# Optimization experiments

Measured on AMD Instinct MI355X. Metric: run time of the kernel, lower is better.

The kernel has to match this reference:

```python
import jax, jax.numpy as jnp
import numpy as np

HEADS = 8
DIM_HEAD = 64
BN_EPS = 1e-5

def setup_inputs() -> dict:
    key = jax.random.key(0)
    ks = jax.random.split(key, 6)
    B, N, D = 8, 1024, 512
    inner = HEADS * DIM_HEAD  # 512
    return {
        "x": jax.random.normal(ks[0], (B, N, D), dtype=jnp.float32),
        "w_qkv": jax.random.normal(ks[1], (D, 3 * inner), dtype=jnp.float32) * (D ** -0.5),
        "conv_w": jax.random.normal(ks[2], (HEADS, HEADS), dtype=jnp.float32) * (HEADS ** -0.5),
        "conv_b": jax.random.normal(ks[3], (HEADS,), dtype=jnp.float32) * 0.02,
        "bn_gamma": jnp.ones((HEADS,), dtype=jnp.float32),
        "bn_beta": jnp.zeros((HEADS,), dtype=jnp.float32),
        "w_out": jax.random.normal(ks[4], (inner, D), dtype=jnp.float32) * (inner ** -0.5),
        "b_out": jnp.zeros((D,), dtype=jnp.float32),
    }

def reference(x, w_qkv, conv_w, conv_b, bn_gamma, bn_beta, w_out, b_out):
    B, N, D = x.shape
    H, dh = HEADS, DIM_HEAD
    scale = dh ** -0.5
    qkv = x @ w_qkv  # [B, N, 3*H*dh]
    q, k, v = jnp.split(qkv, 3, axis=-1)
    # b n (h d) -> b h n d
    q = q.reshape(B, N, H, dh).transpose(0, 2, 1, 3)
    k = k.reshape(B, N, H, dh).transpose(0, 2, 1, 3)
    v = v.reshape(B, N, H, dh).transpose(0, 2, 1, 3)
    attn = jnp.einsum('bhnd,bhmd->bhnm', q, k) * scale
    attn = jax.nn.softmax(attn, axis=-1)
    # 1x1 conv across heads (channels = heads)
    attn = jnp.einsum('gh,bhnm->bgnm', conv_w, attn) + conv_b[None, :, None, None]
    # BatchNorm2d in training mode: batch stats over (B, N, N) per head, biased variance
    mean = attn.mean(axis=(0, 2, 3), keepdims=True)
    var = attn.var(axis=(0, 2, 3), keepdims=True)
    attn = (attn - mean) * jax.lax.rsqrt(var + BN_EPS)
    attn = attn * bn_gamma[None, :, None, None] + bn_beta[None, :, None, None]
    # reatten_scale = 1.0 (transform_scale=False)
    out = jnp.einsum('bhnm,bhmd->bhnd', attn, v)
    out = out.transpose(0, 2, 1, 3).reshape(B, N, H * dh)  # b h n d -> b n (h d)
    return out @ w_out + b_out
```

## Files before the change

kernel.cpp:

```cpp
#include <hip/hip_runtime.h>
#include <math.h>


#define Bz 8
#define Nn 1024
#define Dd 512
#define Hh 8
#define DH 64
#define INNER 512
#define QW 1536
#define SCALE 0.125f
#define BN_EPS 1e-5f

typedef short bf16x8 __attribute__((ext_vector_type(8)));
typedef float f32x4 __attribute__((ext_vector_type(4)));

#define MFMA(a, b, c) __builtin_amdgcn_mfma_f32_16x16x32_bf16((a), (b), (c), 0, 0, 0)

__device__ __forceinline__ unsigned short f2b(float f) {
  union { float f; unsigned u; } v; v.f = f;
  unsigned r = v.u + 0x7fffu + ((v.u >> 16) & 1u);
  return (unsigned short)(r >> 16);
}
__device__ __forceinline__ float b2f(unsigned short s) {
  union { unsigned u; float f; } v; v.u = ((unsigned)s) << 16;
  return v.f;
}

#define WB_QKV 0u
#define WB_VT (WB_QKV + 25165824u)
#define WB_WQT (WB_VT + 8388608u)
#define WB_WOT (WB_WQT + 1572864u)
#define WB_O1 (WB_WOT + 524288u)
#define WB_VSUM (WB_O1 + 16777216u)
#define WB_STATS (WB_VSUM + 16384u)
#define WB_AC (WB_STATS + 64u)

__global__ __launch_bounds__(256) void k_transpose(const float* __restrict__ src,
                                                   unsigned short* __restrict__ dst,
                                                   int R, int C) {
  __shared__ float tile[32][33];
  const int tc = blockIdx.x * 32, tr = blockIdx.y * 32;
  const int lx = threadIdx.x & 31, ly = threadIdx.x >> 5;
#pragma unroll
  for (int i = 0; i < 32; i += 8)
    tile[ly + i][lx] = src[(size_t)(tr + ly + i) * C + tc + lx];
  __syncthreads();
#pragma unroll
  for (int i = 0; i < 32; i += 8)
    dst[(size_t)(tc + ly + i) * R + tr + lx] = f2b(tile[lx][ly + i]);
}

__global__ __launch_bounds__(256) void k_qkv(const float* __restrict__ X,
                                             const unsigned short* __restrict__ WQT,
                                             unsigned short* __restrict__ qkv,
                                             unsigned short* __restrict__ vT) {
  __shared__ unsigned short sA[128][40];
  __shared__ unsigned short sB[128][40];
  const int t = threadIdx.x;
  const int col0 = blockIdx.x * 128;
  const int row0 = blockIdx.y * 128;
  const int l = t & 63, w = t >> 6;
  const int wm = (w & 1) * 64, wn = (w >> 1) * 64;
  const int lm = l & 15, lq = l >> 4;
  const int srow = t >> 1, skc = (t & 1) * 16;
  f32x4 acc[4][4] = {};
  for (int k0 = 0; k0 < Dd; k0 += 32) {
    {
      const float* src = X + (size_t)(row0 + srow) * Dd + k0 + skc;
      unsigned short tmp[16];
#pragma unroll
      for (int c4 = 0; c4 < 4; c4++) {
        float4 f = *(const float4*)(src + c4 * 4);
        tmp[c4 * 4 + 0] = f2b(f.x);
        tmp[c4 * 4 + 1] = f2b(f.y);
        tmp[c4 * 4 + 2] = f2b(f.z);
        tmp[c4 * 4 + 3] = f2b(f.w);
      }
      *(uint4*)&sA[srow][skc] = *(uint4*)tmp;
      *(uint4*)&sA[srow][skc + 8] = *(uint4*)(tmp + 8);
    }
    {
      const unsigned short* srcB = WQT + (size_t)(col0 + srow) * Dd + k0 + skc;
      *(uint4*)&sB[srow][skc] = *(const uint4*)srcB;
      *(uint4*)&sB[srow][skc + 8] = *(const uint4*)(srcB + 8);
    }
    __syncthreads();
    bf16x8 af[4], bfr[4];
#pragma unroll
    for (int i = 0; i < 4; i++) af[i] = *(const bf16x8*)&sA[wm + 16 * i + lm][lq * 8];
#pragma unroll
    for (int j = 0; j < 4; j++) bfr[j] = *(const bf16x8*)&sB[wn + 16 * j + lm][lq * 8];
#pragma unroll
    for (int i = 0; i < 4; i++)
#pragma unroll
      for (int j = 0; j < 4; j++) acc[i][j] = MFMA(af[i], bfr[j], acc[i][j]);
    __syncthreads();
  }
  const bool isv = (col0 >= 2 * INNER);
#pragma unroll
  for (int i = 0; i < 4; i++) {
    const int rbase = row0 + wm + 16 * i + lq * 4;
#pragma unroll
    for (int j = 0; j < 4; j++) {
      const int col = col0 + wn + 16 * j + lm;
#pragma unroll
      for (int r = 0; r < 4; r++) {
        unsigned short hv = f2b(acc[i][j][r]);
        const int row = rbase + r;
        if (!isv) {
          qkv[(size_t)row * QW + col] = hv;
        } else {
          const int b = row >> 10, mseq = row & 1023;
          const int gd = col - 2 * INNER;
          vT[(((size_t)(b * Hh + (gd >> 6))) * DH + (gd & 63)) * Nn + mseq] = hv;
        }
      }
    }
  }
}

__global__ __launch_bounds__(256) void k_vsum(const unsigned short* __restrict__ vT,
                                              float* __restrict__ vsum) {
  const int bg = blockIdx.x;
  const int d = threadIdx.x >> 2, qq = threadIdx.x & 3;
  __shared__ float red[64][4];
  const unsigned short* p = vT + ((size_t)bg * DH + d) * Nn + qq * 256;
  float s = 0.f;
  for (int m = 0; m < 256; m += 4) {
    uint2 rr = *(const uint2*)(p + m);
    s += b2f((unsigned short)(rr.x & 0xffff)) + b2f((unsigned short)(rr.x >> 16)) +
         b2f((unsigned short)(rr.y & 0xffff)) + b2f((unsigned short)(rr.y >> 16));
  }
  red[d][qq] = s;
  __syncthreads();
  if (threadIdx.x < 64)
    vsum[(size_t)bg * DH + threadIdx.x] =
        red[threadIdx.x][0] + red[threadIdx.x][1] + red[threadIdx.x][2] + red[threadIdx.x][3];
}

__global__ __launch_bounds__(512, 2) void k_attn(const unsigned short* __restrict__ qkv,
                                                 const unsigned short* __restrict__ vT,
                                                 const float* __restrict__ conv_w,
                                                 float* __restrict__ O1,
                                                 float* __restrict__ stats) {
  __shared__ unsigned short sQ[8][32][88];
  __shared__ unsigned short sKV[22528];
  __shared__ float sS[8][32][36];
  __shared__ unsigned short sU[8][32][40];
  __shared__ float sRinv[8][32];
  __shared__ float sRed[8][16];
  const int b = blockIdx.x;
  const int n0 = blockIdx.y * 32;
  const int t = threadIdx.x;
  const int w = t >> 6, l = t & 63;
  const int lm = l & 15, lq = l >> 4;
  float cw[64];
#pragma unroll
  for (int i = 0; i < 64; i++) cw[i] = conv_w[i];

  {
    const int row = t >> 1, kc = (t & 1) * 32;
    const int h = row >> 5, n = row & 31;
    const unsigned short* src = qkv + (size_t)(b * Nn + n0 + n) * QW + h * DH + kc;
    uint4 v0 = *(const uint4*)src, v1 = *(const uint4*)(src + 8);
    uint4 v2 = *(const uint4*)(src + 16), v3 = *(const uint4*)(src + 24);
    *(uint4*)&sQ[h][n][kc] = v0;
    *(uint4*)&sQ[h][n][kc + 8] = v1;
    *(uint4*)&sQ[h][n][kc + 16] = v2;
    *(uint4*)&sQ[h][n][kc + 24] = v3;
  }
  __syncthreads();

  float psum[2][4] = {};
  for (int m0 = 0; m0 < Nn; m0 += 32) {
    {
      const int row = t >> 1, kc = (t & 1) * 32;
      const int h = row >> 5, m = row & 31;
      const unsigned short* src = qkv + (size_t)(b * Nn + m0 + m) * QW + INNER + h * DH + kc;
      unsigned short* dst = &sKV[(h * 32 + m) * 88 + kc];
      uint4 v0 = *(const uint4*)src, v1 = *(const uint4*)(src + 8);
      uint4 v2 = *(const uint4*)(src + 16), v3 = *(const uint4*)(src + 24);
      *(uint4*)dst = v0;
      *(uint4*)(dst + 8) = v1;
      *(uint4*)(dst + 16) = v2;
      *(uint4*)(dst + 24) = v3;
    }
    __syncthreads();
    f32x4 lac[2][2] = {};
#pragma unroll
    for (int ks = 0; ks < 2; ks++) {
      bf16x8 a0 = *(const bf16x8*)&sQ[w][lm][ks * 32 + lq * 8];
      bf16x8 a1 = *(const bf16x8*)&sQ[w][16 + lm][ks * 32 + lq * 8];
      bf16x8 b0 = *(const bf16x8*)&sKV[(w * 32 + lm) * 88 + ks * 32 + lq * 8];
      bf16x8 b1 = *(const bf16x8*)&sKV[(w * 32 + 16 + lm) * 88 + ks * 32 + lq * 8];
      lac[0][0] = MFMA(a0, b0, lac[0][0]);
      lac[0][1] = MFMA(a0, b1, lac[0][1]);
      lac[1][0] = MFMA(a1, b0, lac[1][0]);
      lac[1][1] = MFMA(a1, b1, lac[1][1]);
    }
    __syncthreads();
#pragma unroll
    for (int i = 0; i < 2; i++)
#pragma unroll
      for (int j = 0; j < 2; j++)
#pragma unroll
        for (int r = 0; r < 4; r++) psum[i][r] += __expf(lac[i][j][r] * SCALE);
  }
#pragma unroll
  for (int i = 0; i < 2; i++)
#pragma unroll
    for (int r = 0; r < 4; r++) {
      float s = psum[i][r];
      s += __shfl_xor(s, 1);
      s += __shfl_xor(s, 2);
      s += __shfl_xor(s, 4);
      s += __shfl_xor(s, 8);
      if (lm == 0) sRinv[w][16 * i + lq * 4 + r] = 1.0f / s;
    }
  __syncthreads();
  float rv[2][4];
#pragma unroll
  for (int i = 0; i < 2; i++)
#pragma unroll
    for (int r = 0; r < 4; r++) rv[i][r] = sRinv[w][16 * i + lq * 4 + r];

  f32x4 oacc[2][4] = {};
  float su[8] = {}, su2[8] = {};
  const int mxn = t >> 4;
  const int mxm = (t & 15) * 2;
  for (int m0 = 0; m0 < Nn; m0 += 32) {
    {
      const int row = t >> 1, kc = (t & 1) * 32;
      const int h = row >> 5, m = row & 31;
      const unsigned short* src = qkv + (size_t)(b * Nn + m0 + m) * QW + INNER + h * DH + kc;
      unsigned short* dst = &sKV[(h * 32 + m) * 88 + kc];
      uint4 v0 = *(const uint4*)src, v1 = *(const uint4*)(src + 8);
      uint4 v2 = *(const uint4*)(src + 16), v3 = *(const uint4*)(src + 24);
      *(uint4*)dst = v0;
      *(uint4*)(dst + 8) = v1;
      *(uint4*)(dst + 16) = v2;
      *(uint4*)(dst + 24) = v3;
    }
    __syncthreads();
    f32x4 lac[2][2] = {};
#pragma unroll
    for (int ks = 0; ks < 2; ks++) {
      bf16x8 a0 = *(const bf16x8*)&sQ[w][lm][ks * 32 + lq * 8];
      bf16x8 a1 = *(const bf16x8*)&sQ[w][16 + lm][ks * 32 + lq * 8];
      bf16x8 b0 = *(const bf16x8*)&sKV[(w * 32 + lm) * 88 + ks * 32 + lq * 8];
      bf16x8 b1 = *(const bf16x8*)&sKV[(w * 32 + 16 + lm) * 88 + ks * 32 + lq * 8];
      lac[0][0] = MFMA(a0, b0, lac[0][0]);
      lac[0][1] = MFMA(a0, b1, lac[0][1]);
      lac[1][0] = MFMA(a1, b0, lac[1][0]);
      lac[1][1] = MFMA(a1, b1, lac[1][1]);
    }
#pragma unroll
    for (int i = 0; i < 2; i++)
#pragma unroll
      for (int j = 0; j < 2; j++)
#pragma unroll
        for (int r = 0; r < 4; r++)
          sS[w][16 * i + lq * 4 + r][16 * j + lm] = __expf(lac[i][j][r] * SCALE) * rv[i][r];
    __syncthreads();
    {
      const unsigned short* src = vT + ((size_t)(b * Hh + (t >> 6)) * DH + (t & 63)) * Nn + m0;
      unsigned short* dst = &sKV[((t >> 6) * 64 + (t & 63)) * 40];
      uint4 v0 = *(const uint4*)src, v1 = *(const uint4*)(src + 8);
      uint4 v2 = *(const uint4*)(src + 16), v3 = *(const uint4*)(src + 24);
      *(uint4*)dst = v0;
      *(uint4*)(dst + 8) = v1;
      *(uint4*)(dst + 16) = v2;
      *(uint4*)(dst + 24) = v3;
    }
    {
      float2 sv[8];
#pragma unroll
      for (int h = 0; h < 8; h++) sv[h] = *(const float2*)&sS[h][mxn][mxm];
#pragma unroll
      for (int g = 0; g < 8; g++) {
        float u0 = 0.f, u1 = 0.f;
#pragma unroll
        for (int h = 0; h < 8; h++) {
          u0 += cw[g * 8 + h] * sv[h].x;
          u1 += cw[g * 8 + h] * sv[h].y;
        }
        su[g] += u0 + u1;
        su2[g] += u0 * u0 + u1 * u1;
        unsigned pk = (unsigned)f2b(u0) | ((unsigned)f2b(u1) << 16);
        *(unsigned*)&sU[g][mxn][mxm] = pk;
      }
    }
    __syncthreads();
    {
      bf16x8 ua0 = *(const bf16x8*)&sU[w][lm][lq * 8];
      bf16x8 ua1 = *(const bf16x8*)&sU[w][16 + lm][lq * 8];
#pragma unroll
      for (int j = 0; j < 4; j++) {
        bf16x8 vb = *(const bf16x8*)&sKV[(w * 64 + 16 * j + lm) * 40 + lq * 8];
        oacc[0][j] = MFMA(ua0, vb, oacc[0][j]);
        oacc[1][j] = MFMA(ua1, vb, oacc[1][j]);
      }
    }
    __syncthreads();
  }
#pragma unroll
  for (int i = 0; i < 2; i++) {
    const int n = n0 + 16 * i + lq * 4;
#pragma unroll
    for (int j = 0; j < 4; j++) {
      float* dst = O1 + (((size_t)(b * Hh + w)) * Nn + n) * DH + 16 * j + lm;
#pragma unroll
      for (int r = 0; r < 4; r++) dst[(size_t)r * DH] = oacc[i][j][r];
    }
  }
#pragma unroll
  for (int g = 0; g < 8; g++) {
    float a = su[g], q = su2[g];
    for (int off = 32; off; off >>= 1) {
      a += __shfl_down(a, off);
      q += __shfl_down(q, off);
    }
    if (l == 0) {
      sRed[w][g] = a;
      sRed[w][8 + g] = q;
    }
  }
  __syncthreads();
  if (t < 16) {
    float s = 0.f;
#pragma unroll
    for (int ww = 0; ww < 8; ww++) s += sRed[ww][t];
    atomicAdd(&stats[t], s);
  }
}

__global__ void k_alpha(const float* __restrict__ stats, const float* __restrict__ bn_gamma,
                        const float* __restrict__ bn_beta, float* __restrict__ ac) {
  const int g = threadIdx.x;
  if (g < 8) {
    const float cnt = (float)Bz * (float)Nn * (float)Nn;
    float Eu = stats[g] / cnt;
    float Eu2 = stats[8 + g] / cnt;
    float inv = rsqrtf(Eu2 - Eu * Eu + BN_EPS);
    float alpha = bn_gamma[g] * inv;
    ac[g] = alpha;
    ac[8 + g] = bn_beta[g] - Eu * alpha;
  }
}

__global__ __launch_bounds__(256) void k_out(const float* __restrict__ O1,
                                             const float* __restrict__ vsum,
                                             const float* __restrict__ ac,
                                             const unsigned short* __restrict__ WOT,
                                             const float* __restrict__ bout,
                                             float* __restrict__ out) {
  __shared__ unsigned short sA[128][40];
  __shared__ unsigned short sB[128][40];
  __shared__ float sAl[16];
  const int t = threadIdx.x;
  if (t < 16) sAl[t] = ac[t];
  const int col0 = blockIdx.x * 128, row0 = blockIdx.y * 128;
  const int l = t & 63, w = t >> 6;
  const int wm = (w & 1) * 64, wn = (w >> 1) * 64;
  const int lm = l & 15, lq = l >> 4;
  const int srow = t >> 1, skc = (t & 1) * 16;
  const int b = row0 >> 10;
  const int nn = (row0 + srow) & 1023;
  f32x4 acc[4][4] = {};
  __syncthreads();
  for (int k0 = 0; k0 < INNER; k0 += 32) {
    {
      const int k = k0 + skc;
      const int g = k >> 6, dd = k & 63;
      const float al = sAl[g], cc = sAl[8 + g];
      const float* op = O1 + (((size_t)(b * Hh + g)) * Nn + nn) * DH + dd;
      const float* vp = vsum + ((size_t)(b * Hh + g)) * DH + dd;
      unsigned short tmp[16];
#pragma unroll
      for (int c4 = 0; c4 < 4; c4++) {
        float4 o4 = *(const float4*)(op + c4 * 4);
        float4 v4 = *(const float4*)(vp + c4 * 4);
        tmp[c4 * 4 + 0] = f2b(al * o4.x + cc * v4.x);
        tmp[c4 * 4 + 1] = f2b(al * o4.y + cc * v4.y);
        tmp[c4 * 4 + 2] = f2b(al * o4.z + cc * v4.z);
        tmp[c4 * 4 + 3] = f2b(al * o4.w + cc * v4.w);
      }
      *(uint4*)&sA[srow][skc] = *(uint4*)tmp;
      *(uint4*)&sA[srow][skc + 8] = *(uint4*)(tmp + 8);
    }
    {
      const unsigned short* srcB = WOT + (size_t)(col0 + srow) * INNER + k0 + skc;
      *(uint4*)&sB[srow][skc] = *(const uint4*)srcB;
      *(uint4*)&sB[srow][skc + 8] = *(const uint4*)(srcB + 8);
    }
    __syncthreads();
    bf16x8 af[4], bfr[4];
#pragma unroll
    for (int i = 0; i < 4; i++) af[i] = *(const bf16x8*)&sA[wm + 16 * i + lm][lq * 8];
#pragma unroll
    for (int j = 0; j < 4; j++) bfr[j] = *(const bf16x8*)&sB[wn + 16 * j + lm][lq * 8];
#pragma unroll
    for (int i = 0; i < 4; i++)
#pragma unroll
      for (int j = 0; j < 4; j++) acc[i][j] = MFMA(af[i], bfr[j], acc[i][j]);
    __syncthreads();
  }
#pragma unroll
  for (int j = 0; j < 4; j++) {
    const int col = col0 + wn + 16 * j + lm;
    const float bo = bout[col];
#pragma unroll
    for (int i = 0; i < 4; i++) {
      const int rbase = row0 + wm + 16 * i + lq * 4;
#pragma unroll
      for (int r = 0; r < 4; r++) out[(size_t)(rbase + r) * Dd + col] = acc[i][j][r] + bo;
    }
  }
}

extern "C" void kernel_launch(void* const* d_in, const int* in_sizes, int n_in,
                              void* d_out, int out_size, void* d_ws, size_t ws_size,
                              hipStream_t stream) {
  const float* x = (const float*)d_in[0];
  const float* w_qkv = (const float*)d_in[1];
  const float* conv_w = (const float*)d_in[2];
  const float* bn_gamma = (const float*)d_in[4];
  const float* bn_beta = (const float*)d_in[5];
  const float* w_out = (const float*)d_in[6];
  const float* b_out = (const float*)d_in[7];
  char* ws = (char*)d_ws;
  unsigned short* QKV = (unsigned short*)(ws + WB_QKV);
  unsigned short* VT = (unsigned short*)(ws + WB_VT);
  unsigned short* WQT = (unsigned short*)(ws + WB_WQT);
  unsigned short* WOT = (unsigned short*)(ws + WB_WOT);
  float* O1 = (float*)(ws + WB_O1);
  float* VSUM = (float*)(ws + WB_VSUM);
  float* STATS = (float*)(ws + WB_STATS);
  float* AC = (float*)(ws + WB_AC);

  hipMemsetAsync(STATS, 0, 64, stream);
  k_transpose<<<dim3(48, 16), 256, 0, stream>>>(w_qkv, WQT, 512, 1536);
  k_transpose<<<dim3(16, 16), 256, 0, stream>>>(w_out, WOT, 512, 512);
  k_qkv<<<dim3(12, 64), 256, 0, stream>>>(x, WQT, QKV, VT);
  k_vsum<<<64, 256, 0, stream>>>(VT, VSUM);
  k_attn<<<dim3(8, 32), 512, 0, stream>>>(QKV, VT, conv_w, O1, STATS);
  k_alpha<<<1, 64, 0, stream>>>(STATS, bn_gamma, bn_beta, AC);
  k_out<<<dim3(4, 64), 256, 0, stream>>>(O1, VSUM, AC, WOT, b_out, (float*)d_out);
}
```

Baseline: 317.6 us.

## Split attention into score-materializing kernel and head-mixing SV kernel

The fused attention kernel, which computed QK^T twice (once for row sums, once for probabilities), is replaced by two kernels. The first writes unnormalized exp scores in bf16 to a 128MB global buffer together with reciprocal row sums. The second reads those scores, applies the head-mixing conv and accumulates into O1 and the BN statistics. The QKV GEMM epilogue also stages results through shared memory so global stores are coalesced, including the transposed V output. The cost is large global memory traffic for the score buffer in exchange for removing the duplicated QK matmul and getting better occupancy.

```diff
diff --git a/kernel.cpp b/kernel.cpp
--- a/kernel.cpp
+++ b/kernel.cpp
@@ -32,7 +32,9 @@
 #define WB_WQT (WB_VT + 8388608u)
 #define WB_WOT (WB_WQT + 1572864u)
 #define WB_O1 (WB_WOT + 524288u)
-#define WB_VSUM (WB_O1 + 16777216u)
+#define WB_SG (WB_O1 + 16777216u)
+#define WB_RINV (WB_SG + 134217728u)
+#define WB_VSUM (WB_RINV + 262144u)
 #define WB_STATS (WB_VSUM + 16384u)
 #define WB_AC (WB_STATS + 64u)
 
@@ -55,11 +57,14 @@
                                              const unsigned short* __restrict__ WQT,
                                              unsigned short* __restrict__ qkv,
                                              unsigned short* __restrict__ vT) {
-  __shared__ unsigned short sA[128][40];
-  __shared__ unsigned short sB[128][40];
+  extern __shared__ char smem[];
+  unsigned short(*sA)[40] = (unsigned short(*)[40])smem;
+  unsigned short(*sB)[40] = (unsigned short(*)[40])(smem + 128 * 40 * 2);
+  unsigned short* sEp = (unsigned short*)smem;
   const int t = threadIdx.x;
   const int col0 = blockIdx.x * 128;
   const int row0 = blockIdx.y * 128;
+  const bool isqk = (col0 < 2 * INNER);
   const int l = t & 63, w = t >> 6;
   const int wm = (w & 1) * 64, wn = (w >> 1) * 64;
   const int lm = l & 15, lq = l >> 4;
@@ -91,32 +96,54 @@
     for (int i = 0; i < 4; i++) af[i] = *(const bf16x8*)&sA[wm + 16 * i + lm][lq * 8];
 #pragma unroll
     for (int j = 0; j < 4; j++) bfr[j] = *(const bf16x8*)&sB[wn + 16 * j + lm][lq * 8];
-#pragma unroll
-    for (int i = 0; i < 4; i++)
-#pragma unroll
-      for (int j = 0; j < 4; j++) acc[i][j] = MFMA(af[i], bfr[j], acc[i][j]);
-    __syncthreads();
-  }
-  const bool isv = (col0 >= 2 * INNER);
-#pragma unroll
-  for (int i = 0; i < 4; i++) {
-    const int rbase = row0 + wm + 16 * i + lq * 4;
-#pragma unroll
-    for (int j = 0; j < 4; j++) {
-      const int col = col0 + wn + 16 * j + lm;
-#pragma unroll
-      for (int r = 0; r < 4; r++) {
-        unsigned short hv = f2b(acc[i][j][r]);
-        const int row = rbase + r;
-        if (!isv) {
-          qkv[(size_t)row * QW + col] = hv;
-        } else {
-          const int b = row >> 10, mseq = row & 1023;
-          const int gd = col - 2 * INNER;
-          vT[(((size_t)(b * Hh + (gd >> 6))) * DH + (gd & 63)) * Nn + mseq] = hv;
-        }
-      }
-    }
+    if (isqk) {
+#pragma unroll
+      for (int i = 0; i < 4; i++)
+#pragma unroll
+        for (int j = 0; j < 4; j++) acc[i][j] = MFMA(bfr[i], af[j], acc[i][j]);
+    } else {
+#pragma unroll
+      for (int i = 0; i < 4; i++)
+#pragma unroll
+        for (int j = 0; j < 4; j++) acc[i][j] = MFMA(af[i], bfr[j], acc[i][j]);
+    }
+    __syncthreads();
+  }
+  if (isqk) {
+#pragma unroll
+    for (int jc = 0; jc < 4; jc++)
+#pragma unroll
+      for (int ir = 0; ir < 4; ir++) {
+        unsigned short us[4];
+#pragma unroll
+        for (int r = 0; r < 4; r++) us[r] = f2b(acc[jc][ir][r]);
+        *(uint2*)&sEp[(wm + 16 * ir + lm) * 136 + wn + 16 * jc + 4 * lq] = *(uint2*)us;
+      }
+    __syncthreads();
+    const int row = t >> 1, half = t & 1;
+    const unsigned short* src = &sEp[row * 136 + half * 64];
+    unsigned short* dst = qkv + (size_t)(row0 + row) * QW + col0 + half * 64;
+#pragma unroll
+    for (int c = 0; c < 8; c++) *(uint4*)(dst + c * 8) = *(const uint4*)(src + c * 8);
+  } else {
+#pragma unroll
+    for (int ir = 0; ir < 4; ir++)
+#pragma unroll
+      for (int jc = 0; jc < 4; jc++) {
+        unsigned short us[4];
+#pragma unroll
+        for (int r = 0; r < 4; r++) us[r] = f2b(acc[ir][jc][r]);
+        *(uint2*)&sEp[(wn + 16 * jc + lm) * 136 + wm + 16 * ir + 4 * lq] = *(uint2*)us;
+      }
+    __syncthreads();
+    const int row = t >> 1, half = t & 1;
+    const int gd = col0 - 2 * INNER + row;
+    const int bq = row0 >> 10, mseq0 = row0 & 1023;
+    const unsigned short* src = &sEp[row * 136 + half * 64];
+    unsigned short* dst =
+        vT + (((size_t)(bq * Hh + (gd >> 6)) * DH + (gd & 63)) << 10) + mseq0 + half * 64;
+#pragma unroll
+    for (int c = 0; c < 8; c++) *(uint4*)(dst + c * 8) = *(const uint4*)(src + c * 8);
   }
 }
 
@@ -139,181 +166,132 @@
         red[threadIdx.x][0] + red[threadIdx.x][1] + red[threadIdx.x][2] + red[threadIdx.x][3];
 }
 
-__global__ __launch_bounds__(512, 2) void k_attn(const unsigned short* __restrict__ qkv,
-                                                 const unsigned short* __restrict__ vT,
-                                                 const float* __restrict__ conv_w,
-                                                 float* __restrict__ O1,
-                                                 float* __restrict__ stats) {
-  __shared__ unsigned short sQ[8][32][88];
-  __shared__ unsigned short sKV[22528];
-  __shared__ float sS[8][32][36];
-  __shared__ unsigned short sU[8][32][40];
-  __shared__ float sRinv[8][32];
-  __shared__ float sRed[8][16];
-  const int b = blockIdx.x;
-  const int n0 = blockIdx.y * 32;
+__global__ __launch_bounds__(512, 4) void k_sgen(const unsigned short* __restrict__ qkv,
+                                                 unsigned short* __restrict__ Sg,
+                                                 float* __restrict__ rinvG) {
+  __shared__ unsigned short sK[64 * 80];
+  __shared__ unsigned short sSout[128 * 72];
+  const int b = blockIdx.x, ntile = blockIdx.y, h = blockIdx.z;
+  const int n0 = ntile * 128;
   const int t = threadIdx.x;
   const int w = t >> 6, l = t & 63;
   const int lm = l & 15, lq = l >> 4;
+  bf16x8 qf[2];
+  {
+    const unsigned short* qp =
+        qkv + (size_t)(b * Nn + n0 + w * 16 + lm) * QW + h * DH + lq * 8;
+    qf[0] = *(const bf16x8*)(qp);
+    qf[1] = *(const bf16x8*)(qp + 32);
+  }
+  float psum = 0.f;
+  for (int m0 = 0; m0 < Nn; m0 += 64) {
+    {
+      const int row = t >> 3, c = (t & 7) * 8;
+      *(uint4*)&sK[row * 80 + c] =
+          *(const uint4*)(qkv + (size_t)(b * Nn + m0 + row) * QW + INNER + h * DH + c);
+    }
+    __syncthreads();
+    f32x4 lac[4] = {};
+#pragma unroll
+    for (int j = 0; j < 4; j++) {
+      bf16x8 a0 = *(const bf16x8*)&sK[(16 * j + lm) * 80 + lq * 8];
+      bf16x8 a1 = *(const bf16x8*)&sK[(16 * j + lm) * 80 + 32 + lq * 8];
+      lac[j] = MFMA(a0, qf[0], lac[j]);
+      lac[j] = MFMA(a1, qf[1], lac[j]);
+    }
+#pragma unroll
+    for (int j = 0; j < 4; j++) {
+      unsigned short us[4];
+#pragma unroll
+      for (int r = 0; r < 4; r++) {
+        float e = __expf(lac[j][r] * SCALE);
+        psum += e;
+        us[r] = f2b(e);
+      }
+      *(uint2*)&sSout[(w * 16 + lm) * 72 + 16 * j + 4 * lq] = *(uint2*)us;
+    }
+    __syncthreads();
+    {
+      const int row = t >> 2, c = (t & 3) * 16;
+      const unsigned short* src = &sSout[row * 72 + c];
+      unsigned short* dst =
+          Sg + ((size_t)(b * Hh + h) << 20) + (size_t)(n0 + row) * Nn + m0 + c;
+      *(uint4*)dst = *(const uint4*)src;
+      *(uint4*)(dst + 8) = *(const uint4*)(src + 8);
+    }
+  }
+  psum += __shfl_xor(psum, 16);
+  psum += __shfl_xor(psum, 32);
+  if (lq == 0) rinvG[(size_t)(b * Hh + h) * Nn + n0 + w * 16 + lm] = 1.0f / psum;
+}
+
+__global__ __launch_bounds__(512, 4) void k_mixsv(const unsigned short* __restrict__ Sg,
+                                                  const unsigned short* __restrict__ vT,
+                                                  const float* __restrict__ rinvG,
+                                                  const float* __restrict__ conv_w,
+                                                  float* __restrict__ O1,
+                                                  float* __restrict__ stats) {
+  __shared__ unsigned short sU[8 * 16 * 72];
+  __shared__ float sRed[8][16];
+  const int b = blockIdx.x;
+  const int n0 = blockIdx.y * 16;
+  const int t = threadIdx.x;
+  const int w = t >> 6, l = t & 63;
+  const int lm = l & 15, lq = l >> 4;
+  const int mxn = t >> 5, mxm = (t & 31) * 2;
   float cw[64];
 #pragma unroll
   for (int i = 0; i < 64; i++) cw[i] = conv_w[i];
-
-  {
-    const int row = t >> 1, kc = (t & 1) * 32;
-    const int h = row >> 5, n = row & 31;
-    const unsigned short* src = qkv + (size_t)(b * Nn + n0 + n) * QW + h * DH + kc;
-    uint4 v0 = *(const uint4*)src, v1 = *(const uint4*)(src + 8);
-    uint4 v2 = *(const uint4*)(src + 16), v3 = *(const uint4*)(src + 24);
-    *(uint4*)&sQ[h][n][kc] = v0;
-    *(uint4*)&sQ[h][n][kc + 8] = v1;
-    *(uint4*)&sQ[h][n][kc + 16] = v2;
-    *(uint4*)&sQ[h][n][kc + 24] = v3;
-  }
-  __syncthreads();
-
-  float psum[2][4] = {};
-  for (int m0 = 0; m0 < Nn; m0 += 32) {
-    {
-      const int row = t >> 1, kc = (t & 1) * 32;
-      const int h = row >> 5, m = row & 31;
-      const unsigned short* src = qkv + (size_t)(b * Nn + m0 + m) * QW + INNER + h * DH + kc;
-      unsigned short* dst = &sKV[(h * 32 + m) * 88 + kc];
-      uint4 v0 = *(const uint4*)src, v1 = *(const uint4*)(src + 8);
-      uint4 v2 = *(const uint4*)(src + 16), v3 = *(const uint4*)(src + 24);
-      *(uint4*)dst = v0;
-      *(uint4*)(dst + 8) = v1;
-      *(uint4*)(dst + 16) = v2;
-      *(uint4*)(dst + 24) = v3;
-    }
-    __syncthreads();
-    f32x4 lac[2][2] = {};
-#pragma unroll
-    for (int ks = 0; ks < 2; ks++) {
-      bf16x8 a0 = *(const bf16x8*)&sQ[w][lm][ks * 32 + lq * 8];
-      bf16x8 a1 = *(const bf16x8*)&sQ[w][16 + lm][ks * 32 + lq * 8];
-      bf16x8 b0 = *(const bf16x8*)&sKV[(w * 32 + lm) * 88 + ks * 32 + lq * 8];
-      bf16x8 b1 = *(const bf16x8*)&sKV[(w * 32 + 16 + lm) * 88 + ks * 32 + lq * 8];
-      lac[0][0] = MFMA(a0, b0, lac[0][0]);
-      lac[0][1] = MFMA(a0, b1, lac[0][1]);
-      lac[1][0] = MFMA(a1, b0, lac[1][0]);
-      lac[1][1] = MFMA(a1, b1, lac[1][1]);
-    }
-    __syncthreads();
-#pragma unroll
-    for (int i = 0; i < 2; i++)
-#pragma unroll
-      for (int j = 0; j < 2; j++)
-#pragma unroll
-        for (int r = 0; r < 4; r++) psum[i][r] += __expf(lac[i][j][r] * SCALE);
-  }
-#pragma unroll
-  for (int i = 0; i < 2; i++)
-#pragma unroll
-    for (int r = 0; r < 4; r++) {
-      float s = psum[i][r];
-      s += __shfl_xor(s, 1);
-      s += __shfl_xor(s, 2);
-      s += __shfl_xor(s, 4);
-      s += __shfl_xor(s, 8);
-      if (lm == 0) sRinv[w][16 * i + lq * 4 + r] = 1.0f / s;
-    }
-  __syncthreads();
-  float rv[2][4];
-#pragma unroll
-  for (int i = 0; i < 2; i++)
-#pragma unroll
-    for (int r = 0; r < 4; r++) rv[i][r] = sRinv[w][16 * i + lq * 4 + r];
-
-  f32x4 oacc[2][4] = {};
+  float rv[8];
+#pragma unroll
+  for (int h = 0; h < 8; h++) rv[h] = rinvG[(size_t)(b * Hh + h) * Nn + n0 + mxn];
+  f32x4 oacc[4] = {};
   float su[8] = {}, su2[8] = {};
-  const int mxn = t >> 4;
-  const int mxm = (t & 15) * 2;
-  for (int m0 = 0; m0 < Nn; m0 += 32) {
-    {
-      const int row = t >> 1, kc = (t & 1) * 32;
-      const int h = row >> 5, m = row & 31;
-      const unsigned short* src = qkv + (size_t)(b * Nn + m0 + m) * QW + INNER + h * DH + kc;
-      unsigned short* dst = &sKV[(h * 32 + m) * 88 + kc];
-      uint4 v0 = *(const uint4*)src, v1 = *(const uint4*)(src + 8);
-      uint4 v2 = *(const uint4*)(src + 16), v3 = *(const uint4*)(src + 24);
-      *(uint4*)dst = v0;
-      *(uint4*)(dst + 8) = v1;
-      *(uint4*)(dst + 16) = v2;
-      *(uint4*)(dst + 24) = v3;
-    }
-    __syncthreads();
-    f32x4 lac[2][2] = {};
-#pragma unroll
-    for (int ks = 0; ks < 2; ks++) {
-      bf16x8 a0 = *(const bf16x8*)&sQ[w][lm][ks * 32 + lq * 8];
-      bf16x8 a1 = *(const bf16x8*)&sQ[w][16 + lm][ks * 32 + lq * 8];
-      bf16x8 b0 = *(const bf16x8*)&sKV[(w * 32 + lm) * 88 + ks * 32 + lq * 8];
-      bf16x8 b1 = *(const bf16x8*)&sKV[(w * 32 + 16 + lm) * 88 + ks * 32 + lq * 8];
-      lac[0][0] = MFMA(a0, b0, lac[0][0]);
-      lac[0][1] = MFMA(a0, b1, lac[0][1]);
-      lac[1][0] = MFMA(a1, b0, lac[1][0]);
-      lac[1][1] = MFMA(a1, b1, lac[1][1]);
-    }
-#pragma unroll
-    for (int i = 0; i < 2; i++)
-#pragma unroll
-      for (int j = 0; j < 2; j++)
-#pragma unroll
-        for (int r = 0; r < 4; r++)
-          sS[w][16 * i + lq * 4 + r][16 * j + lm] = __expf(lac[i][j][r] * SCALE) * rv[i][r];
-    __syncthreads();
-    {
-      const unsigned short* src = vT + ((size_t)(b * Hh + (t >> 6)) * DH + (t & 63)) * Nn + m0;
-      unsigned short* dst = &sKV[((t >> 6) * 64 + (t & 63)) * 40];
-      uint4 v0 = *(const uint4*)src, v1 = *(const uint4*)(src + 8);
-      uint4 v2 = *(const uint4*)(src + 16), v3 = *(const uint4*)(src + 24);
-      *(uint4*)dst = v0;
-      *(uint4*)(dst + 8) = v1;
-      *(uint4*)(dst + 16) = v2;
-      *(uint4*)(dst + 24) = v3;
-    }
-    {
-      float2 sv[8];
-#pragma unroll
-      for (int h = 0; h < 8; h++) sv[h] = *(const float2*)&sS[h][mxn][mxm];
+  for (int m0 = 0; m0 < Nn; m0 += 64) {
+    {
+      float sx[8], sy[8];
+#pragma unroll
+      for (int h = 0; h < 8; h++) {
+        unsigned pk = *(const unsigned*)(Sg + ((size_t)(b * Hh + h) << 20) +
+                                         (size_t)(n0 + mxn) * Nn + m0 + mxm);
+        sx[h] = b2f((unsigned short)(pk & 0xffff)) * rv[h];
+        sy[h] = b2f((unsigned short)(pk >> 16)) * rv[h];
+      }
 #pragma unroll
       for (int g = 0; g < 8; g++) {
         float u0 = 0.f, u1 = 0.f;
 #pragma unroll
         for (int h = 0; h < 8; h++) {
-          u0 += cw[g * 8 + h] * sv[h].x;
-          u1 += cw[g * 8 + h] * sv[h].y;
+          u0 += cw[g * 8 + h] * sx[h];
+          u1 += cw[g * 8 + h] * sy[h];
         }
         su[g] += u0 + u1;
         su2[g] += u0 * u0 + u1 * u1;
-        unsigned pk = (unsigned)f2b(u0) | ((unsigned)f2b(u1) << 16);
-        *(unsigned*)&sU[g][mxn][mxm] = pk;
-      }
-    }
-    __syncthreads();
-    {
-      bf16x8 ua0 = *(const bf16x8*)&sU[w][lm][lq * 8];
-      bf16x8 ua1 = *(const bf16x8*)&sU[w][16 + lm][lq * 8];
+        *(unsigned*)&sU[(g * 16 + mxn) * 72 + mxm] =
+            (unsigned)f2b(u0) | ((unsigned)f2b(u1) << 16);
+      }
+    }
+    __syncthreads();
+    {
+      bf16x8 uf0 = *(const bf16x8*)&sU[(w * 16 + lm) * 72 + lq * 8];
+      bf16x8 uf1 = *(const bf16x8*)&sU[(w * 16 + lm) * 72 + 32 + lq * 8];
 #pragma unroll
       for (int j = 0; j < 4; j++) {
-        bf16x8 vb = *(const bf16x8*)&sKV[(w * 64 + 16 * j + lm) * 40 + lq * 8];
-        oacc[0][j] = MFMA(ua0, vb, oacc[0][j]);
-        oacc[1][j] = MFMA(ua1, vb, oacc[1][j]);
-      }
-    }
-    __syncthreads();
-  }
-#pragma unroll
-  for (int i = 0; i < 2; i++) {
-    const int n = n0 + 16 * i + lq * 4;
-#pragma unroll
-    for (int j = 0; j < 4; j++) {
-      float* dst = O1 + (((size_t)(b * Hh + w)) * Nn + n) * DH + 16 * j + lm;
-#pragma unroll
-      for (int r = 0; r < 4; r++) dst[(size_t)r * DH] = oacc[i][j][r];
-    }
-  }
+        const unsigned short* vp =
+            vT + (((size_t)(b * Hh + w) * DH + 16 * j + lm) << 10) + m0 + lq * 8;
+        bf16x8 v0 = *(const bf16x8*)vp;
+        bf16x8 v1 = *(const bf16x8*)(vp + 32);
+        oacc[j] = MFMA(uf0, v0, oacc[j]);
+        oacc[j] = MFMA(uf1, v1, oacc[j]);
+      }
+    }
+    __syncthreads();
+  }
+#pragma unroll
+  for (int j = 0; j < 4; j++)
+#pragma unroll
+    for (int r = 0; r < 4; r++)
+      O1[((size_t)(b * Hh + w) * Nn + n0 + lq * 4 + r) * DH + 16 * j + lm] = oacc[j][r];
 #pragma unroll
   for (int g = 0; g < 8; g++) {
     float a = su[g], q = su2[g];
@@ -374,8 +352,8 @@
       const int k = k0 + skc;
       const int g = k >> 6, dd = k & 63;
       const float al = sAl[g], cc = sAl[8 + g];
-      const float* op = O1 + (((size_t)(b * Hh + g)) * Nn + nn) * DH + dd;
-      const float* vp = vsum + ((size_t)(b * Hh + g)) * DH + dd;
+      const float* op = O1 + ((size_t)(b * Hh + g) * Nn + nn) * DH + dd;
+      const float* vp = vsum + (size_t)(b * Hh + g) * DH + dd;
       unsigned short tmp[16];
 #pragma unroll
       for (int c4 = 0; c4 < 4; c4++) {
@@ -435,6 +413,8 @@
   unsigned short* WQT = (unsigned short*)(ws + WB_WQT);
   unsigned short* WOT = (unsigned short*)(ws + WB_WOT);
   float* O1 = (float*)(ws + WB_O1);
+  unsigned short* SG = (unsigned short*)(ws + WB_SG);
+  float* RINV = (float*)(ws + WB_RINV);
   float* VSUM = (float*)(ws + WB_VSUM);
   float* STATS = (float*)(ws + WB_STATS);
   float* AC = (float*)(ws + WB_AC);
@@ -442,9 +422,10 @@
   hipMemsetAsync(STATS, 0, 64, stream);
   k_transpose<<<dim3(48, 16), 256, 0, stream>>>(w_qkv, WQT, 512, 1536);
   k_transpose<<<dim3(16, 16), 256, 0, stream>>>(w_out, WOT, 512, 512);
-  k_qkv<<<dim3(12, 64), 256, 0, stream>>>(x, WQT, QKV, VT);
+  k_qkv<<<dim3(12, 64), 256, 34816, stream>>>(x, WQT, QKV, VT);
   k_vsum<<<64, 256, 0, stream>>>(VT, VSUM);
-  k_attn<<<dim3(8, 32), 512, 0, stream>>>(QKV, VT, conv_w, O1, STATS);
+  k_sgen<<<dim3(8, 8, 8), 512, 0, stream>>>(QKV, SG, RINV);
+  k_mixsv<<<dim3(8, 64), 512, 0, stream>>>(SG, VT, RINV, conv_w, O1, STATS);
   k_alpha<<<1, 64, 0, stream>>>(STATS, bn_gamma, bn_beta, AC);
   k_out<<<dim3(4, 64), 256, 0, stream>>>(O1, VSUM, AC, WOT, b_out, (float*)d_out);
 }
```

After: 277.3 us. -12.7%, faster.
